# Optimization experiments

Hardware: AMD Instinct MI355X
Metric: run time of the kernel (lower is better)

## Reference

```python
import jax, jax.numpy as jnp
import numpy as np

SR = 44100
K = 1.0 / SR                      # time step
LX = 0.5
MAX_OM = 10000.0 * 2.0 * np.pi    # fmax * 2pi
MIN_OM = 20.0 * 2.0 * np.pi
TAU0, TAU1 = 6.0, 1.0
OM2SQ = (2.0 * np.pi * 500.0) ** 2          # OmDamp2^2 (OmDamp1 = 0)
ALPHA = 3.0 * np.log(10.0) / OM2SQ * (OM2SQ / TAU0)   # = 3 ln10 / tau0
BETA = 3.0 * np.log(10.0) / OM2SQ * (1.0 / TAU1 - 1.0 / TAU0)
MU_SCALE, DMU_SCALE, T0MU_SCALE = 2.43, 0.002452, 0.004115
M_MAX = 80  # 80x80 = 6400 modes


def setup_inputs() -> dict:
    z = jnp.zeros((), dtype=jnp.float32)
    return {
        "mu_raw": z, "D_over_mu_raw": z, "T0_over_mu_raw": z,
        "Ly_raw": z, "xo_raw": z, "yo_raw": z,
        "num_samples": 22050,
    }


def _modal_ir(mu_raw, D_over_mu_raw, T0_over_mu_raw, Ly_raw, xo_raw, yo_raw, num_samples):
    sp, sg = jax.nn.softplus, jax.nn.sigmoid
    # physical parameters via differentiable bounds
    mu = (sp(mu_raw) + 1e-4) * MU_SCALE
    D_over_mu = (sp(D_over_mu_raw) + 1e-4) * DMU_SCALE
    T0_over_mu = (sp(T0_over_mu_raw) + 1e-4) * T0MU_SCALE
    Ly = 1.1 + (4.0 - 1.1) * sg(Ly_raw)
    xo = 0.49 * LX + (1.0 - 0.49) * LX * sg(xo_raw)
    yo = 0.51 * Ly + (1.0 - 0.51) * Ly * sg(yo_raw)
    xi = 0.1 * LX
    yi = 0.1 * Ly
    # mode grid [6400]
    idx = jnp.arange(1, M_MAX + 1, dtype=jnp.float32)
    gm, gn = jnp.meshgrid(idx, idx, indexing="ij")
    m, n = gm.ravel(), gn.ravel()
    g1 = (m * np.pi / LX) ** 2 + (n * np.pi / Ly) ** 2
    omega_sq = T0_over_mu * g1 + D_over_mu * g1 * g1
    omega = jnp.sqrt(jax.nn.relu(omega_sq))
    valid = ((omega <= MAX_OM) & (omega >= MIN_OM)).astype(omega.dtype)
    InW = jnp.cos(xi * np.pi * m / LX) * jnp.cos(yi * np.pi * n / Ly)
    OutW = jnp.cos(xo * np.pi * m / LX) * jnp.cos(yo * np.pi * n / Ly)
    sigma = ALPHA + BETA * omega ** 2
    ms = 0.25 * mu * LX * Ly
    P = OutW * InW * (K * K) * jnp.exp(-sigma * K) / ms * valid  # [modes]
    # time axis [T]
    t = jnp.arange(num_samples, dtype=jnp.float32)
    decay_env = jnp.exp(-sigma[:, None] * (t[None, :] - 1.0) * K)    # [modes, T]
    sine_num = jnp.sin(t[None, :] * omega[:, None] * K)              # [modes, T]
    sine_den = jnp.sin(omega * K) + 1e-8                             # [modes]
    mode_waveforms = P[:, None] * decay_env * (sine_num / sine_den[:, None])
    disp = jnp.sum(mode_waveforms, axis=0)                           # [T]
    peak = jnp.max(jnp.abs(disp)) + 1e-8
    return disp / peak


def reference(mu_raw, D_over_mu_raw, T0_over_mu_raw, Ly_raw, xo_raw, yo_raw, num_samples):
    return _modal_ir(mu_raw, D_over_mu_raw, T0_over_mu_raw, Ly_raw, xo_raw, yo_raw, num_samples)
```

## Files before the change

### kernel.cpp

```cpp
#include <hip/hip_runtime.h>
#include <math.h>

#define NMODES 6400
#define TB     128
#define MPT    10
#define NPAIR  5
#define MG     5
#define BATCH  6
#define TC     42

typedef float v2f __attribute__((ext_vector_type(2)));

static __device__ __forceinline__ float softplusf(float x) {
    return log1pf(expf(-fabsf(x))) + fmaxf(x, 0.0f);
}
static __device__ __forceinline__ float sigmoidf(float x) {
    return 1.0f / (1.0f + expf(-x));
}

__global__ void setup_zero_kernel(const float* __restrict__ mu_raw,
                                  const float* __restrict__ Dmu_raw,
                                  const float* __restrict__ T0mu_raw,
                                  const float* __restrict__ Ly_raw,
                                  const float* __restrict__ xo_raw,
                                  const float* __restrict__ yo_raw,
                                  float* __restrict__ wsA,
                                  float* __restrict__ wsW,
                                  float* __restrict__ wsS,
                                  float* __restrict__ wsCW,
                                  float* __restrict__ wsSW,
                                  float* __restrict__ out, int T)
{
    int id = blockIdx.x * blockDim.x + threadIdx.x;
    int gsz = gridDim.x * blockDim.x;
    for (int i = id; i < T; i += gsz) out[i] = 0.0f;
    if (id >= NMODES) return;

    const float KF   = 1.0f / 44100.0f;
    const float PI_F = (float)M_PI;
    const double om2sq = (2.0 * M_PI * 500.0) * (2.0 * M_PI * 500.0);
    const float ALPHA_F  = (float)(3.0 * M_LN10 / om2sq * (om2sq / 6.0));
    const float BETA_F   = (float)(3.0 * M_LN10 / om2sq * (1.0 - 1.0 / 6.0));
    const float MAX_OM_F = (float)(10000.0 * 2.0 * M_PI);
    const float MIN_OM_F = (float)(20.0 * 2.0 * M_PI);
    const float KK_F     = (float)((1.0 / 44100.0) * (1.0 / 44100.0));

    float mu   = (softplusf(mu_raw[0])   + 1e-4f) * 2.43f;
    float Dmu  = (softplusf(Dmu_raw[0])  + 1e-4f) * 0.002452f;
    float T0mu = (softplusf(T0mu_raw[0]) + 1e-4f) * 0.004115f;
    float Ly   = 1.1f + 2.9f * sigmoidf(Ly_raw[0]);
    float xo   = 0.245f + 0.255f * sigmoidf(xo_raw[0]);
    float yo   = __fadd_rn(__fmul_rn(0.51f, Ly),
                           __fmul_rn(__fmul_rn(0.49f, Ly), sigmoidf(yo_raw[0])));

    float mf = (float)(id / 80 + 1);
    float nf = (float)(id % 80 + 1);

    float am = __fmul_rn(__fmul_rn(mf, PI_F), 2.0f);
    float bn = __fdiv_rn(__fmul_rn(nf, PI_F), Ly);
    float g1 = __fadd_rn(__fmul_rn(am, am), __fmul_rn(bn, bn));
    float omega_sq = __fadd_rn(__fmul_rn(T0mu, g1),
                               __fmul_rn(__fmul_rn(Dmu, g1), g1));
    float omega = sqrtf(fmaxf(omega_sq, 0.0f));
    float valid = (omega <= MAX_OM_F && omega >= MIN_OM_F) ? 1.0f : 0.0f;

    float xi_pi = (float)(0.05 * M_PI);
    float yi = __fmul_rn(0.1f, Ly);
    float InW = __fmul_rn(
        cosf(__fmul_rn(__fmul_rn(xi_pi, mf), 2.0f)),
        cosf(__fdiv_rn(__fmul_rn(__fmul_rn(yi, PI_F), nf), Ly)));
    float OutW = __fmul_rn(
        cosf(__fmul_rn(__fmul_rn(__fmul_rn(xo, PI_F), mf), 2.0f)),
        cosf(__fdiv_rn(__fmul_rn(__fmul_rn(yo, PI_F), nf), Ly)));

    float sigma = __fadd_rn(ALPHA_F, __fmul_rn(BETA_F, __fmul_rn(omega, omega)));
    float ms = __fmul_rn(__fmul_rn(__fmul_rn(0.25f, mu), 0.5f), Ly);
    float P = __fmul_rn(
        __fdiv_rn(__fmul_rn(__fmul_rn(__fmul_rn(OutW, InW), KK_F),
                            expf(__fmul_rn(-sigma, KF))),
                  ms),
        valid);
    float den = __fadd_rn(sinf(__fmul_rn(omega, KF)), 1e-8f);
    float A = __fdiv_rn(P, den);

    const double Kd = 1.0 / 44100.0;
    double th = (double)omega * Kd;
    double dd = exp(-(double)sigma * Kd);
    wsA[id]  = A;
    wsW[id]  = omega;
    wsS[id]  = sigma;
    wsCW[id] = (float)(dd * cos(th));
    wsSW[id] = (float)(dd * sin(th));
}

__global__ __launch_bounds__(TB) void accum_kernel(
    const float* __restrict__ wsA,
    const float* __restrict__ wsW,
    const float* __restrict__ wsS,
    const float* __restrict__ wsCW,
    const float* __restrict__ wsSW,
    float* __restrict__ out, int T)
{
    const int tid  = threadIdx.x;
    const int t0   = blockIdx.x * TC;
    const int base = blockIdx.y * (TB * MPT);

    const float  KF     = 1.0f / 44100.0f;
    const double Kd     = 1.0 / 44100.0;
    const double TWO_PI = 6.283185307179586476925286766559;
    const double I2PI   = 0.15915494309189533576888376337251;

    v2f S[NPAIR], C[NPAIR], CW[NPAIR], SW[NPAIR];
    #pragma unroll
    for (int p = 0; p < NPAIR; ++p) {
        int m = base + p * (TB * 2) + tid * 2;
        CW[p] = *(const v2f*)(wsCW + m);
        SW[p] = *(const v2f*)(wsSW + m);
        v2f A  = *(const v2f*)(wsA + m);
        v2f w  = *(const v2f*)(wsW + m);
        v2f sg = *(const v2f*)(wsS + m);
        #pragma unroll
        for (int k = 0; k < 2; ++k) {
            double ph = (double)t0 * (double)w[k] * Kd;
            double q  = rint(ph * I2PI);
            float  r  = (float)fma(-q, TWO_PI, ph);
            float s0, c0;
            __sincosf(r, &s0, &c0);
            float env = A[k] * __expf(-sg[k] * (float)(t0 - 1) * KF);
            S[p][k] = env * s0;
            C[p][k] = env * c0;
        }
    }

    const int lane = tid & 63;

    #pragma unroll 1
    for (int it = 0; it < TC; it += BATCH) {
        float acc[BATCH];
        #pragma unroll
        for (int b = 0; b < BATCH; ++b) {
            v2f s01 = S[0] + S[1];
            v2f s23 = S[2] + S[3];
            v2f sp  = (s01 + s23) + S[4];
            acc[b] = sp[0] + sp[1];
            #pragma unroll
            for (int p = 0; p < NPAIR; ++p) {
                v2f nS = __builtin_elementwise_fma(S[p], CW[p], C[p] * SW[p]);
                v2f nC = __builtin_elementwise_fma(C[p], CW[p], -(S[p] * SW[p]));
                S[p] = nS;
                C[p] = nC;
            }
        }
        #pragma unroll
        for (int off = 32; off > 0; off >>= 1) {
            #pragma unroll
            for (int b = 0; b < BATCH; ++b)
                acc[b] += __shfl_xor(acc[b], off, 64);
        }
        if (lane == 0) {
            int t = t0 + it;
            #pragma unroll
            for (int b = 0; b < BATCH; ++b)
                if (t + b < T) atomicAdd(&out[t + b], acc[b]);
        }
    }
}

__global__ __launch_bounds__(1024) void norm_kernel(float* __restrict__ out, int T)
{
    __shared__ float red[16];
    __shared__ float peakv;
    float mx = 0.0f;
    for (int i = threadIdx.x; i < T; i += 1024) mx = fmaxf(mx, fabsf(out[i]));
    #pragma unroll
    for (int off = 32; off > 0; off >>= 1)
        mx = fmaxf(mx, __shfl_xor(mx, off, 64));
    int lane = threadIdx.x & 63, wv = threadIdx.x >> 6;
    if (lane == 0) red[wv] = mx;
    __syncthreads();
    if (threadIdx.x == 0) {
        float m = red[0];
        #pragma unroll
        for (int i = 1; i < 16; ++i) m = fmaxf(m, red[i]);
        peakv = m + 1e-8f;
    }
    __syncthreads();
    float pk = peakv;
    for (int i = threadIdx.x; i < T; i += 1024) out[i] = __fdiv_rn(out[i], pk);
}

extern "C" void kernel_launch(void* const* d_in, const int* in_sizes, int n_in,
                              void* d_out, int out_size, void* d_ws, size_t ws_size,
                              hipStream_t stream)
{
    const float* mu   = (const float*)d_in[0];
    const float* Dmu  = (const float*)d_in[1];
    const float* T0mu = (const float*)d_in[2];
    const float* Lyr  = (const float*)d_in[3];
    const float* xor_ = (const float*)d_in[4];
    const float* yor_ = (const float*)d_in[5];
    float* out = (float*)d_out;

    float* ws   = (float*)d_ws;
    float* wsA  = ws;
    float* wsW  = ws + NMODES;
    float* wsS  = ws + 2 * NMODES;
    float* wsCW = ws + 3 * NMODES;
    float* wsSW = ws + 4 * NMODES;

    int T = out_size;
    int tchunks = (T + TC - 1) / TC;

    setup_zero_kernel<<<(NMODES + 255) / 256, 256, 0, stream>>>(
        mu, Dmu, T0mu, Lyr, xor_, yor_, wsA, wsW, wsS, wsCW, wsSW, out, T);
    accum_kernel<<<dim3(tchunks, MG), TB, 0, stream>>>(wsA, wsW, wsS, wsCW, wsSW, out, T);
    norm_kernel<<<1, 1024, 0, stream>>>(out, T);
}
```

Measured before the change: 102.0 us.

## Recast modal synthesis as GEMM of chunk states and intra-chunk rotation table

Replaces the per-thread complex-rotation recurrence with a factorization: the setup kernel precomputes, per mode, the 64 intra-chunk powers of the damped rotation and the complex start state of every 64-sample chunk, computed by repeated squaring in double precision. A second kernel then computes each output sample as a dot product over modes of chunk state times intra-chunk power, with the power table staged in LDS. This exposes GEMM-like reuse instead of serial recurrences, but it writes and reads large workspace arrays (about 3.3 MB for the power table and about 18 MB for the chunk states) and moves a long serial double-precision loop into the setup kernel.

```diff
diff --git a/kernel.cpp b/kernel.cpp
--- a/kernel.cpp
+++ b/kernel.cpp
@@ -1,15 +1,12 @@
 #include <hip/hip_runtime.h>
 #include <math.h>
 
-#define NMODES 6400
-#define TB     128
-#define MPT    10
-#define NPAIR  5
-#define MG     5
-#define BATCH  6
-#define TC     42
-
-typedef float v2f __attribute__((ext_vector_type(2)));
+#define NM   6400
+#define DT   64
+#define NC   352
+#define CB   16
+#define MB   64
+#define MGY  100
 
 static __device__ __forceinline__ float softplusf(float x) {
     return log1pf(expf(-fabsf(x))) + fmaxf(x, 0.0f);
@@ -18,23 +15,20 @@
     return 1.0f / (1.0f + expf(-x));
 }
 
-__global__ void setup_zero_kernel(const float* __restrict__ mu_raw,
-                                  const float* __restrict__ Dmu_raw,
-                                  const float* __restrict__ T0mu_raw,
-                                  const float* __restrict__ Ly_raw,
-                                  const float* __restrict__ xo_raw,
-                                  const float* __restrict__ yo_raw,
-                                  float* __restrict__ wsA,
-                                  float* __restrict__ wsW,
-                                  float* __restrict__ wsS,
-                                  float* __restrict__ wsCW,
-                                  float* __restrict__ wsSW,
-                                  float* __restrict__ out, int T)
+__global__ void setup_gen_kernel(const float* __restrict__ mu_raw,
+                                 const float* __restrict__ Dmu_raw,
+                                 const float* __restrict__ T0mu_raw,
+                                 const float* __restrict__ Ly_raw,
+                                 const float* __restrict__ xo_raw,
+                                 const float* __restrict__ yo_raw,
+                                 float2* __restrict__ cdsd,
+                                 float4* __restrict__ statePair,
+                                 float* __restrict__ out, int T)
 {
     int id = blockIdx.x * blockDim.x + threadIdx.x;
     int gsz = gridDim.x * blockDim.x;
     for (int i = id; i < T; i += gsz) out[i] = 0.0f;
-    if (id >= NMODES) return;
+    if (id >= NM) return;
 
     const float KF   = 1.0f / 44100.0f;
     const float PI_F = (float)M_PI;
@@ -44,6 +38,7 @@
     const float MAX_OM_F = (float)(10000.0 * 2.0 * M_PI);
     const float MIN_OM_F = (float)(20.0 * 2.0 * M_PI);
     const float KK_F     = (float)((1.0 / 44100.0) * (1.0 / 44100.0));
+    const double Kd      = 1.0 / 44100.0;
 
     float mu   = (softplusf(mu_raw[0])   + 1e-4f) * 2.43f;
     float Dmu  = (softplusf(Dmu_raw[0])  + 1e-4f) * 0.002452f;
@@ -83,87 +78,107 @@
     float den = __fadd_rn(sinf(__fmul_rn(omega, KF)), 1e-8f);
     float A = __fdiv_rn(P, den);
 
-    const double Kd = 1.0 / 44100.0;
     double th = (double)omega * Kd;
     double dd = exp(-(double)sigma * Kd);
-    wsA[id]  = A;
-    wsW[id]  = omega;
-    wsS[id]  = sigma;
-    wsCW[id] = (float)(dd * cos(th));
-    wsSW[id] = (float)(dd * sin(th));
-}
-
-__global__ __launch_bounds__(TB) void accum_kernel(
-    const float* __restrict__ wsA,
-    const float* __restrict__ wsW,
-    const float* __restrict__ wsS,
-    const float* __restrict__ wsCW,
-    const float* __restrict__ wsSW,
-    float* __restrict__ out, int T)
-{
-    const int tid  = threadIdx.x;
-    const int t0   = blockIdx.x * TC;
-    const int base = blockIdx.y * (TB * MPT);
-
-    const float  KF     = 1.0f / 44100.0f;
-    const double Kd     = 1.0 / 44100.0;
-    const double TWO_PI = 6.283185307179586476925286766559;
-    const double I2PI   = 0.15915494309189533576888376337251;
-
-    v2f S[NPAIR], C[NPAIR], CW[NPAIR], SW[NPAIR];
-    #pragma unroll
-    for (int p = 0; p < NPAIR; ++p) {
-        int m = base + p * (TB * 2) + tid * 2;
-        CW[p] = *(const v2f*)(wsCW + m);
-        SW[p] = *(const v2f*)(wsSW + m);
-        v2f A  = *(const v2f*)(wsA + m);
-        v2f w  = *(const v2f*)(wsW + m);
-        v2f sg = *(const v2f*)(wsS + m);
-        #pragma unroll
-        for (int k = 0; k < 2; ++k) {
-            double ph = (double)t0 * (double)w[k] * Kd;
-            double q  = rint(ph * I2PI);
-            float  r  = (float)fma(-q, TWO_PI, ph);
-            float s0, c0;
-            __sincosf(r, &s0, &c0);
-            float env = A[k] * __expf(-sg[k] * (float)(t0 - 1) * KF);
-            S[p][k] = env * s0;
-            C[p][k] = env * c0;
-        }
-    }
-
-    const int lane = tid & 63;
-
+    double rre = dd * cos(th), rim = dd * sin(th);
+
+    double cre = 1.0, cim = 0.0;
+    float2* cd = cdsd + (size_t)id * DT;
+    #pragma unroll 4
+    for (int dt = 0; dt < DT; ++dt) {
+        cd[dt] = make_float2((float)cre, (float)cim);
+        double nre = cre * rre - cim * rim;
+        double nim = cre * rim + cim * rre;
+        cre = nre; cim = nim;
+    }
+    double R64re = cre, R64im = cim;
+
+    double q_re = R64re, q_im = R64im;
+    double p8re = 0, p8im = 0, p16re = 0, p16im = 0, p64re = 0, p64im = 0;
+    #pragma unroll
+    for (int s = 1; s <= 6; ++s) {
+        double nre = q_re * q_re - q_im * q_im;
+        double nim = 2.0 * q_re * q_im;
+        q_re = nre; q_im = nim;
+        if (s == 3) { p8re = q_re;  p8im = q_im; }
+        if (s == 4) { p16re = q_re; p16im = q_im; }
+        if (s == 6) { p64re = q_re; p64im = q_im; }
+    }
+    double t1re = p64re * p16re - p64im * p16im;
+    double t1im = p64re * p16im + p64im * p16re;
+    double R88re = t1re * p8re - t1im * p8im;
+    double R88im = t1re * p8im + t1im * p8re;
+
+    double z0re = (double)A * exp((double)sigma * Kd), z0im = 0.0;
+    double zr[4], zi[4];
+    zr[0] = z0re; zi[0] = z0im;
+    #pragma unroll
+    for (int k = 1; k < 4; ++k) {
+        zr[k] = zr[k-1] * R88re - zi[k-1] * R88im;
+        zi[k] = zr[k-1] * R88im + zi[k-1] * R88re;
+    }
+
+    float evS[4], evC[4];
     #pragma unroll 1
-    for (int it = 0; it < TC; it += BATCH) {
-        float acc[BATCH];
-        #pragma unroll
-        for (int b = 0; b < BATCH; ++b) {
-            v2f s01 = S[0] + S[1];
-            v2f s23 = S[2] + S[3];
-            v2f sp  = (s01 + s23) + S[4];
-            acc[b] = sp[0] + sp[1];
+    for (int j = 0; j < 88; ++j) {
+        if ((j & 1) == 0) {
             #pragma unroll
-            for (int p = 0; p < NPAIR; ++p) {
-                v2f nS = __builtin_elementwise_fma(S[p], CW[p], C[p] * SW[p]);
-                v2f nC = __builtin_elementwise_fma(C[p], CW[p], -(S[p] * SW[p]));
-                S[p] = nS;
-                C[p] = nC;
+            for (int k = 0; k < 4; ++k) { evS[k] = (float)zi[k]; evC[k] = (float)zr[k]; }
+        } else {
+            #pragma unroll
+            for (int k = 0; k < 4; ++k) {
+                int c = k * 88 + j;
+                statePair[(size_t)(c >> 1) * NM + id] =
+                    make_float4(evS[k], evC[k], (float)zi[k], (float)zr[k]);
             }
         }
         #pragma unroll
-        for (int off = 32; off > 0; off >>= 1) {
-            #pragma unroll
-            for (int b = 0; b < BATCH; ++b)
-                acc[b] += __shfl_xor(acc[b], off, 64);
+        for (int k = 0; k < 4; ++k) {
+            double nre = zr[k] * R64re - zi[k] * R64im;
+            double nim = zr[k] * R64im + zi[k] * R64re;
+            zr[k] = nre; zi[k] = nim;
         }
-        if (lane == 0) {
-            int t = t0 + it;
-            #pragma unroll
-            for (int b = 0; b < BATCH; ++b)
-                if (t + b < T) atomicAdd(&out[t + b], acc[b]);
-        }
-    }
+    }
+}
+
+__global__ __launch_bounds__(256) void gemm_kernel(
+    const float2* __restrict__ cdsd,
+    const float4* __restrict__ statePair,
+    float* __restrict__ out, int T)
+{
+    __shared__ float2 tile[MB * DT];
+    const int tid = threadIdx.x;
+    const int mBase = blockIdx.y * MB;
+
+    const float4* src = (const float4*)(cdsd + (size_t)mBase * DT);
+    float4* dst = (float4*)tile;
+    #pragma unroll
+    for (int i = 0; i < (MB * DT / 2) / 256; ++i)
+        dst[i * 256 + tid] = src[i * 256 + tid];
+    __syncthreads();
+
+    const int wave = tid >> 6, lane = tid & 63;
+    const int c0 = blockIdx.x * CB + wave * 4;
+    const float4* sp0 = statePair + (size_t)(c0 >> 1) * NM + mBase;
+    const float4* sp1 = sp0 + NM;
+
+    float acc0 = 0.0f, acc1 = 0.0f, acc2 = 0.0f, acc3 = 0.0f;
+    #pragma unroll 4
+    for (int m = 0; m < MB; ++m) {
+        float2 w = tile[m * DT + lane];
+        float4 sA = sp0[m];
+        float4 sB = sp1[m];
+        acc0 = __fmaf_rn(sA.x, w.x, acc0); acc0 = __fmaf_rn(sA.y, w.y, acc0);
+        acc1 = __fmaf_rn(sA.z, w.x, acc1); acc1 = __fmaf_rn(sA.w, w.y, acc1);
+        acc2 = __fmaf_rn(sB.x, w.x, acc2); acc2 = __fmaf_rn(sB.y, w.y, acc2);
+        acc3 = __fmaf_rn(sB.z, w.x, acc3); acc3 = __fmaf_rn(sB.w, w.y, acc3);
+    }
+
+    int t = c0 * DT + lane;
+    if (t          < T) atomicAdd(&out[t],          acc0);
+    if (t +     DT < T) atomicAdd(&out[t +     DT], acc1);
+    if (t + 2 * DT < T) atomicAdd(&out[t + 2 * DT], acc2);
+    if (t + 3 * DT < T) atomicAdd(&out[t + 3 * DT], acc3);
 }
 
 __global__ __launch_bounds__(1024) void norm_kernel(float* __restrict__ out, int T)
@@ -201,18 +216,13 @@
     const float* yor_ = (const float*)d_in[5];
     float* out = (float*)d_out;
 
-    float* ws   = (float*)d_ws;
-    float* wsA  = ws;
-    float* wsW  = ws + NMODES;
-    float* wsS  = ws + 2 * NMODES;
-    float* wsCW = ws + 3 * NMODES;
-    float* wsSW = ws + 4 * NMODES;
+    float2* cdsd      = (float2*)d_ws;
+    float4* statePair = (float4*)(cdsd + (size_t)NM * DT);
 
     int T = out_size;
-    int tchunks = (T + TC - 1) / TC;
-
-    setup_zero_kernel<<<(NMODES + 255) / 256, 256, 0, stream>>>(
-        mu, Dmu, T0mu, Lyr, xor_, yor_, wsA, wsW, wsS, wsCW, wsSW, out, T);
-    accum_kernel<<<dim3(tchunks, MG), TB, 0, stream>>>(wsA, wsW, wsS, wsCW, wsSW, out, T);
+
+    setup_gen_kernel<<<(NM + 255) / 256, 256, 0, stream>>>(
+        mu, Dmu, T0mu, Lyr, xor_, yor_, cdsd, statePair, out, T);
+    gemm_kernel<<<dim3(NC / CB, MGY), 256, 0, stream>>>(cdsd, statePair, out, T);
     norm_kernel<<<1, 1024, 0, stream>>>(out, T);
 }
```

After: 137.3 us. +34.6%, slower.
